# Optimization experiments

Hardware: AMD Instinct MI355X
Metric: run time of the kernel (lower is better)

The kernel has to match this reference:

```python
import jax, jax.numpy as jnp
import numpy as np

B, S, D, V, H, L, NM = 16, 512, 768, 30522, 12, 12, 77
HD = D // H  # 64
FF = 4 * D
EPS = 1e-5


def setup_inputs() -> dict:
    key = jax.random.key(0)
    ks = jax.random.split(key, 32)
    sc = 0.02
    n = lambda k, shp: jax.random.normal(k, shp, dtype=jnp.float32) * sc
    d = {}
    d["token_ids"] = jax.random.randint(ks[0], (B, S), 0, V)
    d["segment_ids"] = jax.random.randint(ks[1], (B, S), 0, 2)
    d["mask_ids"] = jax.random.randint(ks[2], (B, NM), 0, S)
    d["tok_emb"] = n(ks[3], (V, D))
    d["pos_emb"] = n(ks[4], (S, D))
    d["seg_emb"] = n(ks[5], (2, D))
    d["dense_w"] = n(ks[6], (V, D))
    d["dense_b"] = jnp.zeros((V,), jnp.float32)
    # per-layer params stacked on leading L axis (torch Linear convention: y = x @ W.T + b)
    d["Wq"] = n(ks[7], (L, D, D)); d["bq"] = jnp.zeros((L, D), jnp.float32)
    d["Wk"] = n(ks[8], (L, D, D)); d["bk"] = jnp.zeros((L, D), jnp.float32)
    d["Wv"] = n(ks[9], (L, D, D)); d["bv"] = jnp.zeros((L, D), jnp.float32)
    d["Wo"] = n(ks[10], (L, D, D)); d["bo"] = jnp.zeros((L, D), jnp.float32)
    d["W1"] = n(ks[11], (L, FF, D)); d["b1"] = jnp.zeros((L, FF), jnp.float32)
    d["W2"] = n(ks[12], (L, D, FF)); d["b2"] = jnp.zeros((L, D), jnp.float32)
    d["g1"] = jnp.ones((L, D), jnp.float32); d["be1"] = jnp.zeros((L, D), jnp.float32)
    d["g2"] = jnp.ones((L, D), jnp.float32); d["be2"] = jnp.zeros((L, D), jnp.float32)
    return d


def _ln(x, g, b):
    m = jnp.mean(x, -1, keepdims=True)
    v = jnp.mean(jnp.square(x - m), -1, keepdims=True)
    return (x - m) * jax.lax.rsqrt(v + EPS) * g + b


def _encoder_stack(x, layer_params):
    def layer(x, p):
        Wq, bq, Wk, bk, Wv, bv, Wo, bo, W1, b1, W2, b2, g1, be1, g2, be2 = p
        q = (x @ Wq.T + bq).reshape(B, S, H, HD).transpose(0, 2, 1, 3)  # bhsd
        k = (x @ Wk.T + bk).reshape(B, S, H, HD).transpose(0, 2, 1, 3)
        v = (x @ Wv.T + bv).reshape(B, S, H, HD).transpose(0, 2, 1, 3)
        scores = jnp.einsum('bhqd,bhkd->bhqk', q, k) / jnp.sqrt(jnp.float32(HD))
        attn = jax.nn.softmax(scores, axis=-1)
        o = jnp.einsum('bhqk,bhkd->bhqd', attn, v).transpose(0, 2, 1, 3).reshape(B, S, D)
        x = _ln(x + (o @ Wo.T + bo), g1, be1)
        h = jax.nn.gelu(x @ W1.T + b1, approximate=False)  # torch nn.GELU default is exact
        h = h @ W2.T + b2
        return _ln(x + h, g2, be2), None
    x, _ = jax.lax.scan(layer, x, layer_params)
    return x


def reference(token_ids, segment_ids, mask_ids, tok_emb, pos_emb, seg_emb,
              dense_w, dense_b, Wq, bq, Wk, bk, Wv, bv, Wo, bo,
              W1, b1, W2, b2, g1, be1, g2, be2):
    x = tok_emb[token_ids] + seg_emb[segment_ids] + pos_emb[None, :, :]  # [B,S,D]
    x = _encoder_stack(x, (Wq, bq, Wk, bk, Wv, bv, Wo, bo, W1, b1, W2, b2, g1, be1, g2, be2))
    idx = jnp.broadcast_to(mask_ids[:, :, None], (B, NM, D))
    out = jnp.take_along_axis(x, idx, axis=1)  # [B,NM,D]
    return out @ dense_w.T + dense_b  # [B,NM,V]
```

## Files before the change

kernel.cpp:

```cpp
#include <hip/hip_runtime.h>
#include <stdint.h>

typedef uint16_t u16;
typedef uint32_t u32;
typedef uint64_t u64;
typedef short short8 __attribute__((ext_vector_type(8)));
typedef float f32x4 __attribute__((ext_vector_type(4)));

#define DEV static __device__ __forceinline__

DEV u16 f2bf(float f){
  u32 x = __builtin_bit_cast(u32, f);
  return (u16)((x + 0x7fffu + ((x >> 16) & 1u)) >> 16);
}

DEV f32x4 mfma16(short8 a, short8 b, f32x4 c){
  return __builtin_amdgcn_mfma_f32_16x16x32_bf16(a, b, c, 0, 0, 0);
}

DEV void async16(const void* g, void* l){
  __builtin_amdgcn_global_load_lds(
      (const __attribute__((address_space(1))) u32*)g,
      (__attribute__((address_space(3))) u32*)l, 16, 0, 0);
}

__global__ __launch_bounds__(256)
void embed_kernel(const int* __restrict__ tid, const int* __restrict__ sid,
                  const float* __restrict__ tok, const float* __restrict__ pos,
                  const float* __restrict__ seg,
                  float* __restrict__ x, u16* __restrict__ xb)
{
  const int row = blockIdx.x;
  const int s = row & 511;
  const int tk = tid[row], sg = sid[row];
  const int t = threadIdx.x;
#pragma unroll
  for (int e = 0; e < 3; ++e){
    int i = t + e*256;
    float v = tok[(u64)tk*768 + i] + seg[(u64)sg*768 + i] + pos[(u64)s*768 + i];
    x[(u64)row*768 + i] = v;
    xb[(u64)row*768 + i] = f2bf(v);
  }
}

__global__ __launch_bounds__(256)
void cvt_bf16(const float4* __restrict__ in, ushort4* __restrict__ out, int n4)
{
  int i = blockIdx.x*256 + threadIdx.x;
  if (i >= n4) return;
  float4 f = in[i];
  ushort4 o;
  o.x = f2bf(f.x); o.y = f2bf(f.y); o.z = f2bf(f.z); o.w = f2bf(f.w);
  out[i] = o;
}

__global__ __launch_bounds__(256)
void cvt_layer(const float4* __restrict__ Wq, const float4* __restrict__ Wk,
               const float4* __restrict__ Wv, const float4* __restrict__ Wo,
               const float4* __restrict__ W1, const float4* __restrict__ W2,
               ushort4* __restrict__ wqkv, ushort4* __restrict__ wob,
               ushort4* __restrict__ w1b, ushort4* __restrict__ w2b)
{
  const int i = blockIdx.x*256 + threadIdx.x;
  const int S = 147456;
  float4 f; ushort4* dst; int di;
  if      (i <   S)       { f = Wq[i];            dst = wqkv; di = i; }
  else if (i < 2*S)       { f = Wk[i - S];        dst = wqkv; di = i; }
  else if (i < 3*S)       { f = Wv[i - 2*S];      dst = wqkv; di = i; }
  else if (i < 4*S)       { f = Wo[i - 3*S];      dst = wob;  di = i - 3*S; }
  else if (i < 4*S+589824){ f = W1[i - 4*S];      dst = w1b;  di = i - 4*S; }
  else                    { f = W2[i - 4*S-589824]; dst = w2b; di = i - 4*S - 589824; }
  ushort4 o;
  o.x = f2bf(f.x); o.y = f2bf(f.y); o.z = f2bf(f.z); o.w = f2bf(f.w);
  dst[di] = o;
}

__global__ __launch_bounds__(256)
void concat_bias(const float* __restrict__ bq, const float* __restrict__ bk,
                 const float* __restrict__ bv, float* __restrict__ out)
{
  const int l = blockIdx.x;
  const int t = threadIdx.x;
#pragma unroll
  for (int e = 0; e < 3; ++e){
    int i = t + e*256;
    out[(u64)l*2304 + i]        = bq[(u64)l*768 + i];
    out[(u64)l*2304 + 768 + i]  = bk[(u64)l*768 + i];
    out[(u64)l*2304 + 1536 + i] = bv[(u64)l*768 + i];
  }
}

DEV void stage128(const u16* __restrict__ X, int ld, int limit,
                  int rowbase, int k0, u16* lds, int t)
{
  const int rl  = t >> 2;
  const int col = (((t & 3) ^ ((t >> 3) & 3))) << 3;
  int r0 = rowbase + rl;       if (r0 > limit-1) r0 = limit-1;
  int r1 = rowbase + rl + 64;  if (r1 > limit-1) r1 = limit-1;
  async16(X + (u64)r0*ld + k0 + col, lds + t*8);
  async16(X + (u64)r1*ld + k0 + col, lds + 2048 + t*8);
}

DEV short8 ldfrag(const u16* buf, int row, int slot){
  return *(const short8*)(buf + row*32 + (slot << 3));
}

template<int EPI>
__global__ __launch_bounds__(256)
void gemm3r(const u16* __restrict__ A, const u16* __restrict__ W,
            const float* __restrict__ bias, void* __restrict__ Cout,
            int M, int N, int Ksp, int ld, int GM, int nsplit, u64 cstride)
{
  __shared__ u16 sm[24576];
  const int t = threadIdx.x;
  const int w = t >> 6, l = t & 63;
  const int lr = l & 15, lg = l >> 4;
  const int wm = (w >> 1)*64, wn = (w & 1)*64;
  const int xr = (lr >> 1) & 3;
  const int slot = lg ^ xr;

  const int nwg = gridDim.x, orig = blockIdx.x;
  const int q = nwg >> 3, r = nwg & 7;
  const int xcd = orig & 7, sl8 = orig >> 3;
  const int wgid = (xcd < r ? xcd*(q+1) : r*(q+1) + (xcd-r)*q) + sl8;
  const int per = nwg / nsplit;
  const int split = wgid / per;
  const int rem = wgid % per;
  const int bm = rem % GM, bn = rem / GM;
  const int koff = split * Ksp;

  f32x4 acc[4][4] = {};
  short8 af[4], bf[4];

  const int NT = Ksp >> 5;
  stage128(A, ld, M, bm*128, koff,      sm,          t);
  stage128(W, ld, N, bn*128, koff,      sm + 4096,   t);
  stage128(A, ld, M, bm*128, koff + 32, sm + 8192,   t);
  stage128(W, ld, N, bn*128, koff + 32, sm + 12288,  t);
  asm volatile("s_waitcnt vmcnt(4)" ::: "memory");
  __builtin_amdgcn_s_barrier();

  for (int tt = 0; tt < NT; ++tt){
    const int rs  = (tt % 3) * 8192;
    const int rs2 = ((tt + 2) % 3) * 8192;
    const int k2  = koff + (tt + 2) * 32;
    const bool st2 = (tt + 2) < NT;
    const u16* Ar = sm + rs;
    const u16* Br = sm + rs + 4096;

    af[0] = ldfrag(Ar, wm + lr, slot);
    af[1] = ldfrag(Ar, wm + 16 + lr, slot);
#pragma unroll
    for (int ni = 0; ni < 4; ++ni) bf[ni] = ldfrag(Br, wn + ni*16 + lr, slot);
    if (st2) stage128(A, ld, M, bm*128, k2, sm + rs2, t);
    __builtin_amdgcn_s_barrier();
    __builtin_amdgcn_s_setprio(1);
#pragma unroll
    for (int mi = 0; mi < 2; ++mi)
#pragma unroll
      for (int ni = 0; ni < 4; ++ni)
        acc[mi][ni] = mfma16(af[mi], bf[ni], acc[mi][ni]);
    __builtin_amdgcn_s_setprio(0);
    __builtin_amdgcn_s_barrier();

    af[2] = ldfrag(Ar, wm + 32 + lr, slot);
    af[3] = ldfrag(Ar, wm + 48 + lr, slot);
    if (st2) stage128(W, ld, N, bn*128, k2, sm + rs2 + 4096, t);
    __builtin_amdgcn_s_barrier();
    __builtin_amdgcn_s_setprio(1);
#pragma unroll
    for (int mi = 2; mi < 4; ++mi)
#pragma unroll
      for (int ni = 0; ni < 4; ++ni)
        acc[mi][ni] = mfma16(af[mi], bf[ni], acc[mi][ni]);
    __builtin_amdgcn_s_setprio(0);
    if (st2) asm volatile("s_waitcnt vmcnt(4)" ::: "memory");
    else     asm volatile("s_waitcnt vmcnt(0)" ::: "memory");
    __builtin_amdgcn_s_barrier();
  }

  __syncthreads();
  constexpr int EPLD = 68;
  float* epw = (float*)sm + w*(16*EPLD);
#pragma unroll
  for (int mi = 0; mi < 4; ++mi){
#pragma unroll
    for (int ni = 0; ni < 4; ++ni){
      int col = bn*128 + wn + ni*16 + lr;
      float bv = (bias && split == 0) ? bias[col < N ? col : N-1] : 0.f;
#pragma unroll
      for (int rr = 0; rr < 4; ++rr){
        float v = acc[mi][ni][rr] + bv;
        if constexpr (EPI == 2) v = 0.5f*v*(1.0f + erff(v*0.70710678118f));
        epw[(lg*4 + rr)*EPLD + ni*16 + lr] = v;
      }
    }
    asm volatile("s_waitcnt lgkmcnt(0)" ::: "memory");
    if constexpr (EPI == 0){
      float* outp = (float*)Cout + (u64)split*cstride;
#pragma unroll
      for (int ps = 0; ps < 4; ++ps){
        int rloc = ps*4 + (l >> 4);
        int row = bm*128 + wm + mi*16 + rloc;
        int col = bn*128 + wn + (l & 15)*4;
        f32x4 v4 = *(const f32x4*)&epw[rloc*EPLD + (l & 15)*4];
        if (row < M){
          if (col + 3 < N) *(f32x4*)(outp + (u64)row*N + col) = v4;
          else {
#pragma unroll
            for (int j = 0; j < 4; ++j)
              if (col + j < N) outp[(u64)row*N + col + j] = v4[j];
          }
        }
      }
    } else {
#pragma unroll
      for (int ps = 0; ps < 2; ++ps){
        int rloc = ps*8 + (l >> 3);
        int row = bm*128 + wm + mi*16 + rloc;
        int col = bn*128 + wn + (l & 7)*8;
        f32x4 a4 = *(const f32x4*)&epw[rloc*EPLD + (l & 7)*8];
        f32x4 b4 = *(const f32x4*)&epw[rloc*EPLD + (l & 7)*8 + 4];
        short8 o8;
        o8[0] = f2bf(a4[0]); o8[1] = f2bf(a4[1]); o8[2] = f2bf(a4[2]); o8[3] = f2bf(a4[3]);
        o8[4] = f2bf(b4[0]); o8[5] = f2bf(b4[1]); o8[6] = f2bf(b4[2]); o8[7] = f2bf(b4[3]);
        if (row < M){
          if (col + 7 < N) *(short8*)((u16*)Cout + (u64)row*N + col) = o8;
          else {
#pragma unroll
            for (int j = 0; j < 8; ++j)
              if (col + j < N) ((u16*)Cout)[(u64)row*N + col + j] = (u16)o8[j];
          }
        }
      }
    }
    asm volatile("s_waitcnt lgkmcnt(0)" ::: "memory");
  }
}

DEV void stage_tile(const u16* __restrict__ X, int ld, int limit,
                    int rowbase, int k0, u16* lds, int t)
{
  const int rl  = t >> 2;
  const int col = (((t & 3) ^ ((t >> 3) & 3))) << 3;
  int r0 = rowbase + rl;        if (r0 > limit-1) r0 = limit-1;
  int r1 = rowbase + rl + 128;  if (r1 > limit-1) r1 = limit-1;
  async16(X + (u64)r0*ld + k0 + col, lds + t*8);
  async16(X + (u64)r1*ld + k0 + col, lds + 4096 + t*8);
}

template<int EPI>
__global__ __launch_bounds__(512)
void gemm8(const u16* __restrict__ A, const u16* __restrict__ W,
           const float* __restrict__ bias, void* __restrict__ Cout,
           int M, int N, int Ksp, int lda, int ldw, int GM, int nsplit,
           u64 cstride)
{
  __shared__ u16 sm[49152];
  u16* Ab = sm;
  u16* Bb = sm + 24576;
  const int t = threadIdx.x;
  const int w = t >> 6, l = t & 63;
  const int lr = l & 15, lg = l >> 4;
  const int wr = w >> 2, wc = w & 3;
  const int xr = (lr >> 1) & 3;
  const int slot = lg ^ xr;

  const int nwg = gridDim.x, orig = blockIdx.x;
  const int q = nwg >> 3, r = nwg & 7;
  const int xcd = orig & 7, sl8 = orig >> 3;
  const int wgid = (xcd < r ? xcd*(q+1) : r*(q+1) + (xcd-r)*q) + sl8;
  const int per = nwg / nsplit;
  const int split = wgid / per;
  const int rem = wgid % per;
  const int bm = rem % GM, bn = rem / GM;
  const int koff = split * Ksp;

  f32x4 acc[8][4] = {};
  short8 afr[4], bfr[4];

  const int NT = Ksp >> 5;
  stage_tile(A, lda, M, bm*256, koff,      Ab,        t);
  stage_tile(W, ldw, N, bn*256, koff,      Bb,        t);
  if (NT > 1){
    stage_tile(A, lda, M, bm*256, koff + 32, Ab + 8192, t);
    stage_tile(W, ldw, N, bn*256, koff + 32, Bb + 8192, t);
  }
  asm volatile("s_waitcnt vmcnt(4)" ::: "memory");
  __builtin_amdgcn_s_barrier();

  for (int tt = 0; tt < NT; ++tt){
    const int rs = (tt % 3) * 8192;
    const int rs2 = ((tt + 2) % 3) * 8192;
    const int k2 = koff + (tt + 2)*32;
    const u16* Ar = Ab + rs;
    const u16* Br = Bb + rs;
#pragma unroll
    for (int mi = 0; mi < 4; ++mi) afr[mi] = ldfrag(Ar, wr*128 + mi*16 + lr, slot);
#pragma unroll
    for (int ni = 0; ni < 4; ++ni) bfr[ni] = ldfrag(Br, wc*64 + ni*16 + lr, slot);
    if (tt + 2 < NT) stage_tile(A, lda, M, bm*256, k2, Ab + rs2, t);
    __builtin_amdgcn_s_barrier();
    __builtin_amdgcn_s_setprio(1);
#pragma unroll
    for (int mi = 0; mi < 4; ++mi)
#pragma unroll
      for (int ni = 0; ni < 4; ++ni)
        acc[mi][ni] = mfma16(afr[mi], bfr[ni], acc[mi][ni]);
    __builtin_amdgcn_s_setprio(0);
    __builtin_amdgcn_s_barrier();
#pragma unroll
    for (int mi = 0; mi < 4; ++mi) afr[mi] = ldfrag(Ar, wr*128 + (mi+4)*16 + lr, slot);
    if (tt + 2 < NT) stage_tile(W, ldw, N, bn*256, k2, Bb + rs2, t);
    __builtin_amdgcn_s_barrier();
    __builtin_amdgcn_s_setprio(1);
#pragma unroll
    for (int mi = 0; mi < 4; ++mi)
#pragma unroll
      for (int ni = 0; ni < 4; ++ni)
        acc[mi+4][ni] = mfma16(afr[mi], bfr[ni], acc[mi+4][ni]);
    __builtin_amdgcn_s_setprio(0);
    if (tt + 2 < NT) asm volatile("s_waitcnt vmcnt(4)" ::: "memory");
    else             asm volatile("s_waitcnt vmcnt(0)" ::: "memory");
    __builtin_amdgcn_s_barrier();
  }

  __syncthreads();
  constexpr int EPLD = 68;
  float* epw = (float*)sm + w*(16*EPLD);
  const int growbase = bm*256 + wr*128;
  const int gcolbase = bn*256 + wc*64;
#pragma unroll
  for (int mi = 0; mi < 8; ++mi){
#pragma unroll
    for (int ni = 0; ni < 4; ++ni){
      int col = gcolbase + ni*16 + lr;
      float bv = (bias && split == 0) ? bias[col < N ? col : N-1] : 0.f;
#pragma unroll
      for (int rr = 0; rr < 4; ++rr){
        float v = acc[mi][ni][rr] + bv;
        if constexpr (EPI == 2) v = 0.5f*v*(1.0f + erff(v*0.70710678118f));
        epw[(lg*4 + rr)*EPLD + ni*16 + lr] = v;
      }
    }
    asm volatile("s_waitcnt lgkmcnt(0)" ::: "memory");
    if constexpr (EPI == 0){
      float* outp = (float*)Cout + (u64)split*cstride;
#pragma unroll
      for (int ps = 0; ps < 4; ++ps){
        int rloc = ps*4 + (l >> 4);
        int row = growbase + mi*16 + rloc;
        int col = gcolbase + (l & 15)*4;
        f32x4 v4 = *(const f32x4*)&epw[rloc*EPLD + (l & 15)*4];
        if (row < M){
          if (col + 3 < N) *(f32x4*)(outp + (u64)row*N + col) = v4;
          else {
#pragma unroll
            for (int j = 0; j < 4; ++j)
              if (col + j < N) outp[(u64)row*N + col + j] = v4[j];
          }
        }
      }
    } else {
#pragma unroll
      for (int ps = 0; ps < 2; ++ps){
        int rloc = ps*8 + (l >> 3);
        int row = growbase + mi*16 + rloc;
        int col = gcolbase + (l & 7)*8;
        f32x4 a4 = *(const f32x4*)&epw[rloc*EPLD + (l & 7)*8];
        f32x4 b4 = *(const f32x4*)&epw[rloc*EPLD + (l & 7)*8 + 4];
        short8 o8;
        o8[0] = f2bf(a4[0]); o8[1] = f2bf(a4[1]); o8[2] = f2bf(a4[2]); o8[3] = f2bf(a4[3]);
        o8[4] = f2bf(b4[0]); o8[5] = f2bf(b4[1]); o8[6] = f2bf(b4[2]); o8[7] = f2bf(b4[3]);
        if (row < M){
          if (col + 7 < N) *(short8*)((u16*)Cout + (u64)row*N + col) = o8;
          else {
#pragma unroll
            for (int j = 0; j < 8; ++j)
              if (col + j < N) ((u16*)Cout)[(u64)row*N + col + j] = (u16)o8[j];
          }
        }
      }
    }
    asm volatile("s_waitcnt lgkmcnt(0)" ::: "memory");
  }
}

__global__ __launch_bounds__(256)
void transpose_v(const u16* __restrict__ qkv, u16* __restrict__ vt)
{
  __shared__ u16 tile[64][72];
  const int st = blockIdx.x, h = blockIdx.y, b = blockIdx.z;
  const int t = threadIdx.x;
#pragma unroll
  for (int e = 0; e < 2; ++e){
    int lin = t + e*256;
    int s = lin >> 3, c8 = (lin & 7)*8;
    *(short8*)(&tile[s][c8]) =
        *(const short8*)(qkv + (u64)(b*512 + st*64 + s)*2304 + 1536 + h*64 + c8);
  }
  __syncthreads();
#pragma unroll
  for (int e = 0; e < 2; ++e){
    int lin = t + e*256;
    int d = lin >> 3, s8 = (lin & 7)*8;
    short8 ov;
#pragma unroll
    for (int i = 0; i < 8; ++i) ov[i] = (short)tile[s8 + i][d];
    *(short8*)(vt + ((u64)(b*12 + h)*64 + d)*512 + st*64 + s8) = ov;
  }
}

__global__ __launch_bounds__(256)
void attn_kernel(const u16* __restrict__ qkv, const u16* __restrict__ vt,
                 u16* __restrict__ ob)
{
  __shared__ u16 p_lds[4][16][72];
  const int t = threadIdx.x, w = t >> 6, ll = t & 63;
  const int lr = ll & 15, lg = ll >> 4;
  const int qt = blockIdx.x, h = blockIdx.y, b = blockIdx.z;
  const int q0 = qt*64 + w*16;
  const float C = 0.125f * 1.44269504f;

  const u16* qrow = qkv + (u64)(b*512 + q0 + lr)*2304 + h*64 + 8*lg;
  const short8 qf0 = *(const short8*)qrow;
  const short8 qf1 = *(const short8*)(qrow + 32);

  const u16* kbh = qkv + (u64)(b*512)*2304 + 768 + h*64;
  const u16* vth = vt + (u64)(b*12 + h)*64*512;

  f32x4 lacc = {0.f, 0.f, 0.f, 0.f};
  f32x4 o_acc[4] = {};

  for (int jt = 0; jt < 8; ++jt){
    const int jb = jt*64;
    f32x4 s[4] = {};
#pragma unroll
    for (int jn = 0; jn < 4; ++jn){
      const u16* kr = kbh + (u64)(jb + jn*16 + lr)*2304 + 8*lg;
      short8 kf0 = *(const short8*)kr;
      short8 kf1 = *(const short8*)(kr + 32);
      s[jn] = mfma16(qf0, kf0, s[jn]);
      s[jn] = mfma16(qf1, kf1, s[jn]);
    }
#pragma unroll
    for (int jn = 0; jn < 4; ++jn)
#pragma unroll
      for (int r = 0; r < 4; ++r){
        float pv = exp2f(s[jn][r]*C);
        s[jn][r] = pv;
        lacc[r] += pv;
      }
#pragma unroll
    for (int jn = 0; jn < 4; ++jn)
#pragma unroll
      for (int r = 0; r < 4; ++r)
        p_lds[w][4*lg + r][jn*16 + lr] = f2bf(s[jn][r]);
    asm volatile("s_waitcnt lgkmcnt(0)" ::: "memory");
    short8 pa0 = *(const short8*)(&p_lds[w][lr][8*lg]);
    short8 pa1 = *(const short8*)(&p_lds[w][lr][32 + 8*lg]);
#pragma unroll
    for (int nd = 0; nd < 4; ++nd){
      const u16* vr = vth + (u64)(nd*16 + lr)*512 + jb + 8*lg;
      short8 vf0 = *(const short8*)vr;
      short8 vf1 = *(const short8*)(vr + 32);
      o_acc[nd] = mfma16(pa0, vf0, o_acc[nd]);
      o_acc[nd] = mfma16(pa1, vf1, o_acc[nd]);
    }
    asm volatile("s_waitcnt lgkmcnt(0)" ::: "memory");
  }
  float l_r[4];
#pragma unroll
  for (int r = 0; r < 4; ++r){
    float v = lacc[r];
#pragma unroll
    for (int m = 1; m < 16; m <<= 1) v += __shfl_xor(v, m);
    l_r[r] = 1.f / v;
  }
#pragma unroll
  for (int nd = 0; nd < 4; ++nd)
#pragma unroll
    for (int r = 0; r < 4; ++r)
      p_lds[w][4*lg + r][nd*16 + lr] = f2bf(o_acc[nd][r]*l_r[r]);
  asm volatile("s_waitcnt lgkmcnt(0)" ::: "memory");
#pragma unroll
  for (int ps = 0; ps < 2; ++ps){
    int row = ps*8 + (ll >> 3);
    short8 ov = *(const short8*)(&p_lds[w][row][(ll & 7)*8]);
    *(short8*)(ob + (u64)(b*512 + q0 + row)*768 + h*64 + (ll & 7)*8) = ov;
  }
}

__global__ __launch_bounds__(256)
void ln_res(const float* xin, const float* __restrict__ yin, u64 cstride, int nsplit,
            const float* __restrict__ g, const float* __restrict__ be,
            float* xout, u16* __restrict__ xbout)
{
  __shared__ float sred[8];
  const int row = blockIdx.x, t = threadIdx.x;
  const int w = t >> 6, ll = t & 63;
  float v[3]; float s = 0.f, sq = 0.f;
#pragma unroll
  for (int e = 0; e < 3; ++e){
    int i = t + e*256;
    float val = xin[(u64)row*768 + i];
    for (int sp = 0; sp < nsplit; ++sp)
      val += yin[(u64)sp*cstride + (u64)row*768 + i];
    v[e] = val; s += val; sq += val*val;
  }
#pragma unroll
  for (int m = 1; m < 64; m <<= 1){ s += __shfl_xor(s, m); sq += __shfl_xor(sq, m); }
  if (ll == 0){ sred[w] = s; sred[4 + w] = sq; }
  __syncthreads();
  s  = sred[0] + sred[1] + sred[2] + sred[3];
  sq = sred[4] + sred[5] + sred[6] + sred[7];
  const float mean = s*(1.f/768.f);
  const float rstd = rsqrtf(sq*(1.f/768.f) - mean*mean + 1e-5f);
#pragma unroll
  for (int e = 0; e < 3; ++e){
    int i = t + e*256;
    float o = (v[e] - mean)*rstd*g[i] + be[i];
    xout[(u64)row*768 + i] = o;
    xbout[(u64)row*768 + i] = f2bf(o);
  }
}

__global__ __launch_bounds__(256)
void gather_rows(const u16* __restrict__ xb, const int* __restrict__ mids,
                 u16* __restrict__ xg)
{
  const int row = blockIdx.x;
  const int b = row / 77;
  const int src = b*512 + mids[row];
  const int t = threadIdx.x;
#pragma unroll
  for (int e = 0; e < 3; ++e){
    int i = t + e*256;
    xg[(u64)row*768 + i] = xb[(u64)src*768 + i];
  }
}

extern "C" void kernel_launch(void* const* d_in, const int* in_sizes, int n_in,
                              void* d_out, int out_size, void* d_ws, size_t ws_size,
                              hipStream_t stream)
{
  const int*   token_ids  = (const int*)  d_in[0];
  const int*   segment_ids= (const int*)  d_in[1];
  const int*   mask_ids   = (const int*)  d_in[2];
  const float* tok_emb    = (const float*)d_in[3];
  const float* pos_emb    = (const float*)d_in[4];
  const float* seg_emb    = (const float*)d_in[5];
  const float* dense_w    = (const float*)d_in[6];
  const float* dense_b    = (const float*)d_in[7];
  const float* Wq = (const float*)d_in[8];  const float* bq = (const float*)d_in[9];
  const float* Wk = (const float*)d_in[10]; const float* bk = (const float*)d_in[11];
  const float* Wv = (const float*)d_in[12]; const float* bv = (const float*)d_in[13];
  const float* Wo = (const float*)d_in[14]; const float* bo = (const float*)d_in[15];
  const float* W1 = (const float*)d_in[16]; const float* b1 = (const float*)d_in[17];
  const float* W2 = (const float*)d_in[18]; const float* b2 = (const float*)d_in[19];
  const float* g1 = (const float*)d_in[20]; const float* be1= (const float*)d_in[21];
  const float* g2 = (const float*)d_in[22]; const float* be2= (const float*)d_in[23];

  char* p = (char*)d_ws;
  auto alloc = [&](size_t bytes)->char*{
    char* r = p; p += (bytes + 255) & ~(size_t)255; return r;
  };
  const u64 T = 8192;
  float* x    = (float*)alloc(T*768*4);
  float* y    = (float*)alloc(T*768*4);
  u16*   xb   = (u16*)  alloc(T*768*2);
  u16*   qkvb = (u16*)  alloc(T*2304*2);
  u16*   vT   = (u16*)  alloc(T*768*2);
  u16*   obuf = (u16*)  alloc(T*768*2);
  u16*   h1b  = (u16*)  alloc(T*3072*2);
  u16*   xg   = (u16*)  alloc((u64)1232*768*2);
  u16*   wqkv = (u16*)  alloc((u64)2304*768*2);
  u16*   wob  = (u16*)  alloc((u64)768*768*2);
  u16*   w1b  = (u16*)  alloc((u64)3072*768*2);
  u16*   w2b  = (u16*)  alloc((u64)3072*768*2);
  float* bqkv = (float*)alloc((u64)12*2304*4);
  u16*   dwb  = h1b;

  if ((size_t)(p - (char*)d_ws) > ws_size) return;

  const u64 CSTR = (u64)((float*)(void*)qkvb - y);

  embed_kernel<<<dim3(8192), dim3(256), 0, stream>>>(
      token_ids, segment_ids, tok_emb, pos_emb, seg_emb, x, xb);
  concat_bias<<<dim3(12), dim3(256), 0, stream>>>(bq, bk, bv, bqkv);

  for (int l = 0; l < 12; ++l){
    cvt_layer<<<dim3(6912), dim3(256), 0, stream>>>(
        (const float4*)(Wq + (u64)l*589824), (const float4*)(Wk + (u64)l*589824),
        (const float4*)(Wv + (u64)l*589824), (const float4*)(Wo + (u64)l*589824),
        (const float4*)(W1 + (u64)l*2359296), (const float4*)(W2 + (u64)l*2359296),
        (ushort4*)wqkv, (ushort4*)wob, (ushort4*)w1b, (ushort4*)w2b);

    gemm3r<1><<<dim3(64*18), dim3(256), 0, stream>>>(xb, wqkv, bqkv + (u64)l*2304, qkvb,
                                                     8192, 2304, 768, 768, 64, 1, 0);

    transpose_v<<<dim3(8, 12, 16), dim3(256), 0, stream>>>(qkvb, vT);
    attn_kernel<<<dim3(8, 12, 16), dim3(256), 0, stream>>>(qkvb, vT, obuf);

    gemm3r<0><<<dim3(64*6*2), dim3(256), 0, stream>>>(obuf, wob, bo + (u64)l*768, y,
                                                      8192, 768, 384, 768, 64, 2, CSTR);
    ln_res<<<dim3(8192), dim3(256), 0, stream>>>(x, y, CSTR, 2, g1 + (u64)l*768, be1 + (u64)l*768, x, xb);

    gemm3r<2><<<dim3(64*24), dim3(256), 0, stream>>>(xb, w1b, b1 + (u64)l*3072, h1b,
                                                     8192, 3072, 768, 768, 64, 1, 0);
    gemm3r<0><<<dim3(64*6*2), dim3(256), 0, stream>>>(h1b, w2b, b2 + (u64)l*768, y,
                                                      8192, 768, 1536, 3072, 64, 2, CSTR);
    ln_res<<<dim3(8192), dim3(256), 0, stream>>>(x, y, CSTR, 2, g2 + (u64)l*768, be2 + (u64)l*768, x, xb);
  }

  gather_rows<<<dim3(1232), dim3(256), 0, stream>>>(xb, mask_ids, xg);
  cvt_bf16<<<dim3(22892), dim3(256), 0, stream>>>((const float4*)dense_w, (ushort4*)dwb, 5860224);
  gemm8<0><<<dim3(5*120), dim3(512), 0, stream>>>(xg, dwb, dense_b, (float*)d_out,
                                                  1232, 30522, 768, 768, 768, 5, 1, 0);
}
```

Before: 4.238 ms.

## Fuse residual add into GEMM epilogue, drop split-K and fp32 residual stream

The Wo and W2 GEMMs now run without split-K and add the bf16 residual (xb) in their epilogue, writing one fp32 buffer. The layernorm kernel then reads only that buffer, and the separate fp32 residual copy x is removed from embed and layernorm. This cuts memory traffic for the second split partial and the fp32 residual read/write. The cost is half as many workgroups for the N=768 GEMMs and a residual carried in bf16 rather than fp32, which lowers accuracy.

```diff
diff --git a/kernel.cpp b/kernel.cpp
--- a/kernel.cpp
+++ b/kernel.cpp
@@ -14,6 +14,11 @@
   return (u16)((x + 0x7fffu + ((x >> 16) & 1u)) >> 16);
 }
 
+DEV float bf2f(u16 u){
+  u32 v = (u32)u << 16;
+  return __builtin_bit_cast(float, v);
+}
+
 DEV f32x4 mfma16(short8 a, short8 b, f32x4 c){
   return __builtin_amdgcn_mfma_f32_16x16x32_bf16(a, b, c, 0, 0, 0);
 }
@@ -27,8 +32,7 @@
 __global__ __launch_bounds__(256)
 void embed_kernel(const int* __restrict__ tid, const int* __restrict__ sid,
                   const float* __restrict__ tok, const float* __restrict__ pos,
-                  const float* __restrict__ seg,
-                  float* __restrict__ x, u16* __restrict__ xb)
+                  const float* __restrict__ seg, u16* __restrict__ xb)
 {
   const int row = blockIdx.x;
   const int s = row & 511;
@@ -38,7 +42,6 @@
   for (int e = 0; e < 3; ++e){
     int i = t + e*256;
     float v = tok[(u64)tk*768 + i] + seg[(u64)sg*768 + i] + pos[(u64)s*768 + i];
-    x[(u64)row*768 + i] = v;
     xb[(u64)row*768 + i] = f2bf(v);
   }
 }
@@ -108,8 +111,8 @@
 template<int EPI>
 __global__ __launch_bounds__(256)
 void gemm3r(const u16* __restrict__ A, const u16* __restrict__ W,
-            const float* __restrict__ bias, void* __restrict__ Cout,
-            int M, int N, int Ksp, int ld, int GM, int nsplit, u64 cstride)
+            const float* __restrict__ bias, const u16* __restrict__ xres,
+            void* __restrict__ Cout, int M, int N, int K, int GM)
 {
   __shared__ u16 sm[24576];
   const int t = threadIdx.x;
@@ -123,27 +126,23 @@
   const int q = nwg >> 3, r = nwg & 7;
   const int xcd = orig & 7, sl8 = orig >> 3;
   const int wgid = (xcd < r ? xcd*(q+1) : r*(q+1) + (xcd-r)*q) + sl8;
-  const int per = nwg / nsplit;
-  const int split = wgid / per;
-  const int rem = wgid % per;
-  const int bm = rem % GM, bn = rem / GM;
-  const int koff = split * Ksp;
+  const int bm = wgid % GM, bn = wgid / GM;
 
   f32x4 acc[4][4] = {};
   short8 af[4], bf[4];
 
-  const int NT = Ksp >> 5;
-  stage128(A, ld, M, bm*128, koff,      sm,          t);
-  stage128(W, ld, N, bn*128, koff,      sm + 4096,   t);
-  stage128(A, ld, M, bm*128, koff + 32, sm + 8192,   t);
-  stage128(W, ld, N, bn*128, koff + 32, sm + 12288,  t);
+  const int NT = K >> 5;
+  stage128(A, K, M, bm*128,  0, sm,          t);
+  stage128(W, K, N, bn*128,  0, sm + 4096,   t);
+  stage128(A, K, M, bm*128, 32, sm + 8192,   t);
+  stage128(W, K, N, bn*128, 32, sm + 12288,  t);
   asm volatile("s_waitcnt vmcnt(4)" ::: "memory");
   __builtin_amdgcn_s_barrier();
 
   for (int tt = 0; tt < NT; ++tt){
     const int rs  = (tt % 3) * 8192;
     const int rs2 = ((tt + 2) % 3) * 8192;
-    const int k2  = koff + (tt + 2) * 32;
+    const int k2  = (tt + 2) * 32;
     const bool st2 = (tt + 2) < NT;
     const u16* Ar = sm + rs;
     const u16* Br = sm + rs + 4096;
@@ -152,7 +151,7 @@
     af[1] = ldfrag(Ar, wm + 16 + lr, slot);
 #pragma unroll
     for (int ni = 0; ni < 4; ++ni) bf[ni] = ldfrag(Br, wn + ni*16 + lr, slot);
-    if (st2) stage128(A, ld, M, bm*128, k2, sm + rs2, t);
+    if (st2) stage128(A, K, M, bm*128, k2, sm + rs2, t);
     __builtin_amdgcn_s_barrier();
     __builtin_amdgcn_s_setprio(1);
 #pragma unroll
@@ -165,7 +164,7 @@
 
     af[2] = ldfrag(Ar, wm + 32 + lr, slot);
     af[3] = ldfrag(Ar, wm + 48 + lr, slot);
-    if (st2) stage128(W, ld, N, bn*128, k2, sm + rs2 + 4096, t);
+    if (st2) stage128(W, K, N, bn*128, k2, sm + rs2 + 4096, t);
     __builtin_amdgcn_s_barrier();
     __builtin_amdgcn_s_setprio(1);
 #pragma unroll
@@ -187,7 +186,7 @@
 #pragma unroll
     for (int ni = 0; ni < 4; ++ni){
       int col = bn*128 + wn + ni*16 + lr;
-      float bv = (bias && split == 0) ? bias[col < N ? col : N-1] : 0.f;
+      float bv = bias ? bias[col < N ? col : N-1] : 0.f;
 #pragma unroll
       for (int rr = 0; rr < 4; ++rr){
         float v = acc[mi][ni][rr] + bv;
@@ -197,7 +196,6 @@
     }
     asm volatile("s_waitcnt lgkmcnt(0)" ::: "memory");
     if constexpr (EPI == 0){
-      float* outp = (float*)Cout + (u64)split*cstride;
 #pragma unroll
       for (int ps = 0; ps < 4; ++ps){
         int rloc = ps*4 + (l >> 4);
@@ -205,11 +203,21 @@
         int col = bn*128 + wn + (l & 15)*4;
         f32x4 v4 = *(const f32x4*)&epw[rloc*EPLD + (l & 15)*4];
         if (row < M){
-          if (col + 3 < N) *(f32x4*)(outp + (u64)row*N + col) = v4;
-          else {
+          if (col + 3 < N){
+            if (xres){
+              ushort4 x4 = *(const ushort4*)(xres + (u64)row*N + col);
+              v4[0] += bf2f(x4.x); v4[1] += bf2f(x4.y);
+              v4[2] += bf2f(x4.z); v4[3] += bf2f(x4.w);
+            }
+            *(f32x4*)((float*)Cout + (u64)row*N + col) = v4;
+          } else {
 #pragma unroll
             for (int j = 0; j < 4; ++j)
-              if (col + j < N) outp[(u64)row*N + col + j] = v4[j];
+              if (col + j < N){
+                float vv = v4[j];
+                if (xres) vv += bf2f(xres[(u64)row*N + col + j]);
+                ((float*)Cout)[(u64)row*N + col + j] = vv;
+              }
           }
         }
       }
@@ -249,12 +257,10 @@
   async16(X + (u64)r1*ld + k0 + col, lds + 4096 + t*8);
 }
 
-template<int EPI>
 __global__ __launch_bounds__(512)
-void gemm8(const u16* __restrict__ A, const u16* __restrict__ W,
-           const float* __restrict__ bias, void* __restrict__ Cout,
-           int M, int N, int Ksp, int lda, int ldw, int GM, int nsplit,
-           u64 cstride)
+void gemm8v(const u16* __restrict__ A, const u16* __restrict__ W,
+            const float* __restrict__ bias, float* __restrict__ Cout,
+            int M, int N, int K, int GM)
 {
   __shared__ u16 sm[49152];
   u16* Ab = sm;
@@ -270,36 +276,30 @@
   const int q = nwg >> 3, r = nwg & 7;
   const int xcd = orig & 7, sl8 = orig >> 3;
   const int wgid = (xcd < r ? xcd*(q+1) : r*(q+1) + (xcd-r)*q) + sl8;
-  const int per = nwg / nsplit;
-  const int split = wgid / per;
-  const int rem = wgid % per;
-  const int bm = rem % GM, bn = rem / GM;
-  const int koff = split * Ksp;
+  const int bm = wgid % GM, bn = wgid / GM;
 
   f32x4 acc[8][4] = {};
   short8 afr[4], bfr[4];
 
-  const int NT = Ksp >> 5;
-  stage_tile(A, lda, M, bm*256, koff,      Ab,        t);
-  stage_tile(W, ldw, N, bn*256, koff,      Bb,        t);
-  if (NT > 1){
-    stage_tile(A, lda, M, bm*256, koff + 32, Ab + 8192, t);
-    stage_tile(W, ldw, N, bn*256, koff + 32, Bb + 8192, t);
-  }
+  const int NT = K >> 5;
+  stage_tile(A, K, M, bm*256,  0, Ab,        t);
+  stage_tile(W, K, N, bn*256,  0, Bb,        t);
+  stage_tile(A, K, M, bm*256, 32, Ab + 8192, t);
+  stage_tile(W, K, N, bn*256, 32, Bb + 8192, t);
   asm volatile("s_waitcnt vmcnt(4)" ::: "memory");
   __builtin_amdgcn_s_barrier();
 
   for (int tt = 0; tt < NT; ++tt){
     const int rs = (tt % 3) * 8192;
     const int rs2 = ((tt + 2) % 3) * 8192;
-    const int k2 = koff + (tt + 2)*32;
+    const int k2 = (tt + 2)*32;
     const u16* Ar = Ab + rs;
     const u16* Br = Bb + rs;
 #pragma unroll
     for (int mi = 0; mi < 4; ++mi) afr[mi] = ldfrag(Ar, wr*128 + mi*16 + lr, slot);
 #pragma unroll
     for (int ni = 0; ni < 4; ++ni) bfr[ni] = ldfrag(Br, wc*64 + ni*16 + lr, slot);
-    if (tt + 2 < NT) stage_tile(A, lda, M, bm*256, k2, Ab + rs2, t);
+    if (tt + 2 < NT) stage_tile(A, K, M, bm*256, k2, Ab + rs2, t);
     __builtin_amdgcn_s_barrier();
     __builtin_amdgcn_s_setprio(1);
 #pragma unroll
@@ -311,7 +311,7 @@
     __builtin_amdgcn_s_barrier();
 #pragma unroll
     for (int mi = 0; mi < 4; ++mi) afr[mi] = ldfrag(Ar, wr*128 + (mi+4)*16 + lr, slot);
-    if (tt + 2 < NT) stage_tile(W, ldw, N, bn*256, k2, Bb + rs2, t);
+    if (tt + 2 < NT) stage_tile(W, K, N, bn*256, k2, Bb + rs2, t);
     __builtin_amdgcn_s_barrier();
     __builtin_amdgcn_s_setprio(1);
 #pragma unroll
@@ -335,50 +335,24 @@
 #pragma unroll
     for (int ni = 0; ni < 4; ++ni){
       int col = gcolbase + ni*16 + lr;
-      float bv = (bias && split == 0) ? bias[col < N ? col : N-1] : 0.f;
-#pragma unroll
-      for (int rr = 0; rr < 4; ++rr){
-        float v = acc[mi][ni][rr] + bv;
-        if constexpr (EPI == 2) v = 0.5f*v*(1.0f + erff(v*0.70710678118f));
-        epw[(lg*4 + rr)*EPLD + ni*16 + lr] = v;
-      }
+      float bv = bias ? bias[col < N ? col : N-1] : 0.f;
+#pragma unroll
+      for (int rr = 0; rr < 4; ++rr)
+        epw[(lg*4 + rr)*EPLD + ni*16 + lr] = acc[mi][ni][rr] + bv;
     }
     asm volatile("s_waitcnt lgkmcnt(0)" ::: "memory");
-    if constexpr (EPI == 0){
-      float* outp = (float*)Cout + (u64)split*cstride;
-#pragma unroll
-      for (int ps = 0; ps < 4; ++ps){
-        int rloc = ps*4 + (l >> 4);
-        int row = growbase + mi*16 + rloc;
-        int col = gcolbase + (l & 15)*4;
-        f32x4 v4 = *(const f32x4*)&epw[rloc*EPLD + (l & 15)*4];
-        if (row < M){
-          if (col + 3 < N) *(f32x4*)(outp + (u64)row*N + col) = v4;
-          else {
-#pragma unroll
-            for (int j = 0; j < 4; ++j)
-              if (col + j < N) outp[(u64)row*N + col + j] = v4[j];
-          }
-        }
-      }
-    } else {
-#pragma unroll
-      for (int ps = 0; ps < 2; ++ps){
-        int rloc = ps*8 + (l >> 3);
-        int row = growbase + mi*16 + rloc;
-        int col = gcolbase + (l & 7)*8;
-        f32x4 a4 = *(const f32x4*)&epw[rloc*EPLD + (l & 7)*8];
-        f32x4 b4 = *(const f32x4*)&epw[rloc*EPLD + (l & 7)*8 + 4];
-        short8 o8;
-        o8[0] = f2bf(a4[0]); o8[1] = f2bf(a4[1]); o8[2] = f2bf(a4[2]); o8[3] = f2bf(a4[3]);
-        o8[4] = f2bf(b4[0]); o8[5] = f2bf(b4[1]); o8[6] = f2bf(b4[2]); o8[7] = f2bf(b4[3]);
-        if (row < M){
-          if (col + 7 < N) *(short8*)((u16*)Cout + (u64)row*N + col) = o8;
-          else {
-#pragma unroll
-            for (int j = 0; j < 8; ++j)
-              if (col + j < N) ((u16*)Cout)[(u64)row*N + col + j] = (u16)o8[j];
-          }
+#pragma unroll
+    for (int ps = 0; ps < 4; ++ps){
+      int rloc = ps*4 + (l >> 4);
+      int row = growbase + mi*16 + rloc;
+      int col = gcolbase + (l & 15)*4;
+      f32x4 v4 = *(const f32x4*)&epw[rloc*EPLD + (l & 15)*4];
+      if (row < M){
+        if (col + 3 < N) *(f32x4*)(Cout + (u64)row*N + col) = v4;
+        else {
+#pragma unroll
+          for (int j = 0; j < 4; ++j)
+            if (col + j < N) Cout[(u64)row*N + col + j] = v4[j];
         }
       }
     }
@@ -492,9 +466,9 @@
 }
 
 __global__ __launch_bounds__(256)
-void ln_res(const float* xin, const float* __restrict__ yin, u64 cstride, int nsplit,
-            const float* __restrict__ g, const float* __restrict__ be,
-            float* xout, u16* __restrict__ xbout)
+void ln_only(const float* __restrict__ yin,
+             const float* __restrict__ g, const float* __restrict__ be,
+             u16* __restrict__ xbout)
 {
   __shared__ float sred[8];
   const int row = blockIdx.x, t = threadIdx.x;
@@ -503,9 +477,7 @@
 #pragma unroll
   for (int e = 0; e < 3; ++e){
     int i = t + e*256;
-    float val = xin[(u64)row*768 + i];
-    for (int sp = 0; sp < nsplit; ++sp)
-      val += yin[(u64)sp*cstride + (u64)row*768 + i];
+    float val = yin[(u64)row*768 + i];
     v[e] = val; s += val; sq += val*val;
   }
 #pragma unroll
@@ -519,9 +491,7 @@
 #pragma unroll
   for (int e = 0; e < 3; ++e){
     int i = t + e*256;
-    float o = (v[e] - mean)*rstd*g[i] + be[i];
-    xout[(u64)row*768 + i] = o;
-    xbout[(u64)row*768 + i] = f2bf(o);
+    xbout[(u64)row*768 + i] = f2bf((v[e] - mean)*rstd*g[i] + be[i]);
   }
 }
 
@@ -566,7 +536,6 @@
     char* r = p; p += (bytes + 255) & ~(size_t)255; return r;
   };
   const u64 T = 8192;
-  float* x    = (float*)alloc(T*768*4);
   float* y    = (float*)alloc(T*768*4);
   u16*   xb   = (u16*)  alloc(T*768*2);
   u16*   qkvb = (u16*)  alloc(T*2304*2);
@@ -583,10 +552,8 @@
 
   if ((size_t)(p - (char*)d_ws) > ws_size) return;
 
-  const u64 CSTR = (u64)((float*)(void*)qkvb - y);
-
   embed_kernel<<<dim3(8192), dim3(256), 0, stream>>>(
-      token_ids, segment_ids, tok_emb, pos_emb, seg_emb, x, xb);
+      token_ids, segment_ids, tok_emb, pos_emb, seg_emb, xb);
   concat_bias<<<dim3(12), dim3(256), 0, stream>>>(bq, bk, bv, bqkv);
 
   for (int l = 0; l < 12; ++l){
@@ -596,25 +563,25 @@
         (const float4*)(W1 + (u64)l*2359296), (const float4*)(W2 + (u64)l*2359296),
         (ushort4*)wqkv, (ushort4*)wob, (ushort4*)w1b, (ushort4*)w2b);
 
-    gemm3r<1><<<dim3(64*18), dim3(256), 0, stream>>>(xb, wqkv, bqkv + (u64)l*2304, qkvb,
-                                                     8192, 2304, 768, 768, 64, 1, 0);
+    gemm3r<1><<<dim3(64*18), dim3(256), 0, stream>>>(xb, wqkv, bqkv + (u64)l*2304, nullptr,
+                                                     qkvb, 8192, 2304, 768, 64);
 
     transpose_v<<<dim3(8, 12, 16), dim3(256), 0, stream>>>(qkvb, vT);
     attn_kernel<<<dim3(8, 12, 16), dim3(256), 0, stream>>>(qkvb, vT, obuf);
 
-    gemm3r<0><<<dim3(64*6*2), dim3(256), 0, stream>>>(obuf, wob, bo + (u64)l*768, y,
-                                                      8192, 768, 384, 768, 64, 2, CSTR);
-    ln_res<<<dim3(8192), dim3(256), 0, stream>>>(x, y, CSTR, 2, g1 + (u64)l*768, be1 + (u64)l*768, x, xb);
-
-    gemm3r<2><<<dim3(64*24), dim3(256), 0, stream>>>(xb, w1b, b1 + (u64)l*3072, h1b,
-                                                     8192, 3072, 768, 768, 64, 1, 0);
-    gemm3r<0><<<dim3(64*6*2), dim3(256), 0, stream>>>(h1b, w2b, b2 + (u64)l*768, y,
-                                                      8192, 768, 1536, 3072, 64, 2, CSTR);
-    ln_res<<<dim3(8192), dim3(256), 0, stream>>>(x, y, CSTR, 2, g2 + (u64)l*768, be2 + (u64)l*768, x, xb);
+    gemm3r<0><<<dim3(64*6), dim3(256), 0, stream>>>(obuf, wob, bo + (u64)l*768, xb,
+                                                    y, 8192, 768, 768, 64);
+    ln_only<<<dim3(8192), dim3(256), 0, stream>>>(y, g1 + (u64)l*768, be1 + (u64)l*768, xb);
+
+    gemm3r<2><<<dim3(64*24), dim3(256), 0, stream>>>(xb, w1b, b1 + (u64)l*3072, nullptr,
+                                                     h1b, 8192, 3072, 768, 64);
+    gemm3r<0><<<dim3(64*6), dim3(256), 0, stream>>>(h1b, w2b, b2 + (u64)l*768, xb,
+                                                    y, 8192, 768, 3072, 64);
+    ln_only<<<dim3(8192), dim3(256), 0, stream>>>(y, g2 + (u64)l*768, be2 + (u64)l*768, xb);
   }
 
   gather_rows<<<dim3(1232), dim3(256), 0, stream>>>(xb, mask_ids, xg);
   cvt_bf16<<<dim3(22892), dim3(256), 0, stream>>>((const float4*)dense_w, (ushort4*)dwb, 5860224);
-  gemm8<0><<<dim3(5*120), dim3(512), 0, stream>>>(xg, dwb, dense_b, (float*)d_out,
-                                                  1232, 30522, 768, 768, 768, 5, 1, 0);
-}
+  gemm8v<<<dim3(5*120), dim3(512), 0, stream>>>(xg, dwb, dense_b, (float*)d_out,
+                                                1232, 30522, 768, 5);
+}
```

New measurement: 4.205 ms. Within noise of the previous version (-0.8%).
